# Kernel tuning notes

Measured on AMD Instinct MI355X. Metric: run time of the kernel, lower is better.

## Reference

```python
import jax, jax.numpy as jnp
import numpy as np

B, T, D, H = 64, 512, 512, 1024


def setup_inputs() -> dict:
    key = jax.random.key(0)
    k_x, k_m, k_wi, k_wh = jax.random.split(key, 4)
    x = jax.random.normal(k_x, (B, T, D), dtype=jnp.float32)
    mask = jax.random.randint(k_m, (B, T), 0, 2, dtype=jnp.int32)
    # LSTMCell params: xavier_uniform for W_ih, orthogonal for W_hh, zero biases
    lim = float(np.sqrt(6.0 / (4 * H + D)))
    W_ih = jax.random.uniform(k_wi, (4 * H, D), dtype=jnp.float32, minval=-lim, maxval=lim)
    A = jax.random.normal(k_wh, (4 * H, H), dtype=jnp.float32)
    Q, _ = jnp.linalg.qr(A.T)  # (H, 4H) columns orthonormal -> rows of W_hh orthogonal-ish per torch init
    W_hh = Q.T.astype(jnp.float32)
    W_hh = jnp.concatenate([W_hh] * ((4 * H) // W_hh.shape[0]), axis=0)[: 4 * H]
    b_ih = jnp.zeros((4 * H,), dtype=jnp.float32)
    b_hh = jnp.zeros((4 * H,), dtype=jnp.float32)
    h0 = jnp.zeros((1, H), dtype=jnp.float32)
    c0 = jnp.zeros((1, H), dtype=jnp.float32)
    return {"x": x, "mask": mask, "W_ih": W_ih, "W_hh": W_hh,
            "b_ih": b_ih, "b_hh": b_hh, "h0": h0, "c0": c0}


def reference(x, mask, W_ih, W_hh, b_ih, b_hh, h0, c0):
    Bn, Tn, _ = x.shape
    Hn = h0.shape[1]
    # Precompute input projection for all timesteps: (B, T, 4H)
    xg = jnp.einsum('btd,gd->btg', x, W_ih) + b_ih + b_hh

    def step(carry, inp):
        h, c = carry
        xg_t, m_t = inp  # (B, 4H), (B,)
        gates = xg_t + h @ W_hh.T  # (B, 4H)
        i, f, g, o = jnp.split(gates, 4, axis=-1)  # torch LSTMCell gate order i,f,g,o
        i = jax.nn.sigmoid(i)
        f = jax.nn.sigmoid(f)
        g = jnp.tanh(g)
        o = jax.nn.sigmoid(o)
        c_new = f * c + i * g
        h_new = o * jnp.tanh(c_new)
        keep = (m_t != 0)[:, None]
        h2 = jnp.where(keep, h_new, h)
        c2 = jnp.where(keep, c_new, c)
        return (h2, c2), h2

    h_init = jnp.broadcast_to(h0, (Bn, Hn))
    c_init = jnp.broadcast_to(c0, (Bn, Hn))
    xs = (jnp.swapaxes(xg, 0, 1), mask.T)  # time-major for scan
    (_, _), hs = jax.lax.scan(step, (h_init, c_init), xs)
    return jnp.swapaxes(hs, 0, 1)  # (B, T, H)
```

## Files before the change

kernel.cpp:

```cpp
#include <hip/hip_runtime.h>

#define B_   64
#define T_   512
#define D_   512
#define H_   1024
#define G4   4096
#define KC_N 48

typedef float f32x4 __attribute__((ext_vector_type(4)));
typedef short s16x8 __attribute__((ext_vector_type(8)));

__device__ __forceinline__ unsigned short f2bf(float f) {
    unsigned int u = __float_as_uint(f);
    u = (u + 0x7fffu + ((u >> 16) & 1u)) >> 16;
    return (unsigned short)u;
}
__device__ __forceinline__ float sigm(float x) { return 1.f / (1.f + __expf(-x)); }
__device__ __forceinline__ float tanh_f(float x) { return 1.f - 2.f / (__expf(2.f * x) + 1.f); }

__device__ __forceinline__ s16x8 cvt8(float4 a, float4 b) {
    union { s16x8 v; unsigned int u[4]; } r;
    asm("v_cvt_pk_bf16_f32 %0, %1, %2" : "=v"(r.u[0]) : "v"(a.x), "v"(a.y));
    asm("v_cvt_pk_bf16_f32 %0, %1, %2" : "=v"(r.u[1]) : "v"(a.z), "v"(a.w));
    asm("v_cvt_pk_bf16_f32 %0, %1, %2" : "=v"(r.u[2]) : "v"(b.x), "v"(b.y));
    asm("v_cvt_pk_bf16_f32 %0, %1, %2" : "=v"(r.u[3]) : "v"(b.z), "v"(b.w));
    return r.v;
}

__global__ __launch_bounds__(256) void pack_w(const float* __restrict__ W_ih,
                                              const float* __restrict__ W_hh,
                                              unsigned short* __restrict__ Wpk) {
    int tid = blockIdx.x * 256 + threadIdx.x;
    int j    = tid & 7;
    int lane = (tid >> 3) & 63;
    int rest = tid >> 9;
    int kc = rest % KC_N;
    int c  = rest / KC_N;
    int npk = c * 16 + (lane & 15);
    int jh = npk >> 2, g = npk & 3;
    int row = g * H_ + jh;
    int k = kc * 32 + (lane >> 4) * 8 + j;
    float v = (k < D_) ? W_ih[row * D_ + k] : W_hh[row * H_ + (k - D_)];
    Wpk[tid] = f2bf(v);
}

__global__ __launch_bounds__(256) void init_state2(
    const float* __restrict__ h0, const float* __restrict__ b_ih,
    const float* __restrict__ b_hh, unsigned short* __restrict__ hbuf,
    float* __restrict__ bias_p, unsigned int* __restrict__ flags)
{
    int tid = blockIdx.x * 256 + threadIdx.x;
    int j = tid & (H_ - 1);
    hbuf[tid] = f2bf(h0[j]);
    if (tid < G4) {
        int jh = tid >> 2, g = tid & 3;
        bias_p[tid] = b_ih[g * H_ + jh] + b_hh[g * H_ + jh];
    }
    if (tid < 256) flags[tid] = 0u;
}

__global__ __launch_bounds__(512) void lstm_persist(
    const float* __restrict__ x, const int* __restrict__ mask,
    const unsigned short* __restrict__ Wpk, const float* __restrict__ bias_p,
    const float* __restrict__ h0, const float* __restrict__ c0,
    unsigned short* __restrict__ hbuf, float* __restrict__ out,
    unsigned int* __restrict__ flags)
{
    const int tid = threadIdx.x;
    const int bid = blockIdx.x;
    const int cg  = bid >> 1;
    const int mh  = bid & 1;
    const int b0g = mh << 5;

    const int w = tid >> 6, l = tid & 63;
    const int quad = l >> 4, l15 = l & 15;
    const int mi = w >> 2;
    const int ks = w & 3;
    const int arow = b0g + mi * 16 + l15;

    __shared__ float Dls[4][32][36];

    s16x8 Bf0[12], Bf1[12];
    {
        const unsigned short* base0 = Wpk + (size_t)((cg * 2 + 0) * KC_N) * 512;
        const unsigned short* base1 = Wpk + (size_t)((cg * 2 + 1) * KC_N) * 512;
        #pragma unroll
        for (int i = 0; i < 12; ++i) {
            int kc = (i < 4) ? (ks * 4 + i) : (16 + ks * 8 + (i - 4));
            Bf0[i] = *reinterpret_cast<const s16x8*>(base0 + ((size_t)kc * 64 + l) * 8);
            Bf1[i] = *reinterpret_cast<const s16x8*>(base1 + ((size_t)kc * 64 + l) * 8);
        }
        #pragma unroll
        for (int i = 0; i < 12; ++i)
            asm volatile("" : "+v"(Bf0[i]), "+v"(Bf1[i]));
    }

    const int b_l = tid >> 3, u = tid & 7;
    const int brow = b0g + b_l;
    const int jcol = cg * 8 + u;
    float c_reg = 0.f, h_reg = 0.f;
    float4 bias = make_float4(0.f, 0.f, 0.f, 0.f);
    if (tid < 256) {
        c_reg = c0[jcol];
        h_reg = h0[jcol];
        bias = *reinterpret_cast<const float4*>(bias_p + cg * 32 + u * 4);
    }

    unsigned int* myflag = flags + mh * 128 + cg;
    const unsigned long long* pollp =
        reinterpret_cast<const unsigned long long*>(flags + mh * 128) + l;
    const float* xbase = x + (size_t)arow * T_ * D_ + ks * 128 + quad * 8;

    #pragma unroll 1
    for (int t = 0; t < T_; ++t) {
        const unsigned short* hin  = hbuf + (size_t)(t & 1) * (B_ * H_);
        unsigned short*       hout = hbuf + (size_t)((t + 1) & 1) * (B_ * H_);

        f32x4 a0 = {0.f, 0.f, 0.f, 0.f}, a1 = {0.f, 0.f, 0.f, 0.f};
        const float* xp = xbase + (size_t)t * D_;
        int mv = 0;
        if (tid < 256) mv = mask[(size_t)brow * T_ + t];
        #pragma unroll
        for (int i = 0; i < 4; ++i) {
            float4 v0 = *reinterpret_cast<const float4*>(xp + i * 32);
            float4 v1 = *reinterpret_cast<const float4*>(xp + i * 32 + 4);
            s16x8 af = cvt8(v0, v1);
            a0 = __builtin_amdgcn_mfma_f32_16x16x32_bf16(af, Bf0[i], a0, 0, 0, 0);
            a1 = __builtin_amdgcn_mfma_f32_16x16x32_bf16(af, Bf1[i], a1, 0, 0, 0);
        }

        if (t > 0 && w == 0) {
            const unsigned int tgt = (unsigned int)t;
            int guard = 0;
            for (;;) {
                unsigned long long v = __hip_atomic_load(pollp, __ATOMIC_RELAXED,
                                                         __HIP_MEMORY_SCOPE_AGENT);
                int ok = ((unsigned int)v >= tgt) && ((unsigned int)(v >> 32) >= tgt);
                if (__all(ok)) break;
                __builtin_amdgcn_s_sleep(2);
                if (++guard > (1 << 16)) break;
            }
        }
        __builtin_amdgcn_s_barrier();
        __builtin_amdgcn_fence(__ATOMIC_ACQUIRE, "workgroup");

        const unsigned short* hrow = hin + (size_t)arow * H_ + ks * 256 + quad * 8;
        s16x8 hf[8];
        #pragma unroll
        for (int i = 0; i < 8; ++i) {
            const unsigned long long* hp =
                reinterpret_cast<const unsigned long long*>(hrow + i * 32);
            union { s16x8 v; unsigned long long q[2]; } au;
            au.q[0] = __hip_atomic_load(hp,     __ATOMIC_RELAXED, __HIP_MEMORY_SCOPE_AGENT);
            au.q[1] = __hip_atomic_load(hp + 1, __ATOMIC_RELAXED, __HIP_MEMORY_SCOPE_AGENT);
            hf[i] = au.v;
        }
        #pragma unroll
        for (int i = 0; i < 8; ++i) {
            a0 = __builtin_amdgcn_mfma_f32_16x16x32_bf16(hf[i], Bf0[4 + i], a0, 0, 0, 0);
            a1 = __builtin_amdgcn_mfma_f32_16x16x32_bf16(hf[i], Bf1[4 + i], a1, 0, 0, 0);
        }
        #pragma unroll
        for (int r = 0; r < 4; ++r) {
            Dls[ks][mi * 16 + quad * 4 + r][l15]      = a0[r];
            Dls[ks][mi * 16 + quad * 4 + r][16 + l15] = a1[r];
        }
        __syncthreads();

        float h2s = 0.f;
        if (tid < 256) {
            f32x4 s0 = *reinterpret_cast<f32x4*>(&Dls[0][b_l][u * 4]);
            f32x4 s1 = *reinterpret_cast<f32x4*>(&Dls[1][b_l][u * 4]);
            f32x4 s2 = *reinterpret_cast<f32x4*>(&Dls[2][b_l][u * 4]);
            f32x4 s3 = *reinterpret_cast<f32x4*>(&Dls[3][b_l][u * 4]);
            f32x4 g = s0 + s1 + s2 + s3;
            float gi = sigm  (g[0] + bias.x);
            float gf = sigm  (g[1] + bias.y);
            float gg = tanh_f(g[2] + bias.z);
            float go = sigm  (g[3] + bias.w);
            float c_new = gf * c_reg + gi * gg;
            float h_new = go * tanh_f(c_new);
            float h2 = mv ? h_new : h_reg;
            c_reg = mv ? c_new : c_reg;
            h_reg = h2;
            h2s = h2;
            unsigned int hv = (unsigned int)f2bf(h2);
            unsigned int hx = (unsigned int)__shfl_xor((int)hv, 1);
            if ((u & 1) == 0) {
                unsigned int pk = (hx << 16) | hv;
                __hip_atomic_store(reinterpret_cast<unsigned int*>(
                                       hout + (size_t)brow * H_ + jcol),
                                   pk, __ATOMIC_RELAXED, __HIP_MEMORY_SCOPE_AGENT);
            }
        }
        __syncthreads();

        if (t < T_ - 1 && tid == 0)
            __hip_atomic_store(myflag, (unsigned int)(t + 1),
                               __ATOMIC_RELAXED, __HIP_MEMORY_SCOPE_AGENT);
        if (tid < 256)
            out[((size_t)brow * T_ + t) * H_ + jcol] = h2s;
    }
}

extern "C" void kernel_launch(void* const* d_in, const int* in_sizes, int n_in,
                              void* d_out, int out_size, void* d_ws, size_t ws_size,
                              hipStream_t stream)
{
    const float* x    = (const float*)d_in[0];
    const int*   mask = (const int*)d_in[1];
    const float* W_ih = (const float*)d_in[2];
    const float* W_hh = (const float*)d_in[3];
    const float* b_ih = (const float*)d_in[4];
    const float* b_hh = (const float*)d_in[5];
    const float* h0   = (const float*)d_in[6];
    const float* c0   = (const float*)d_in[7];
    float* out = (float*)d_out;

    char* wsb = (char*)d_ws;
    unsigned short* Wpk    = (unsigned short*)(wsb);
    float*          bias_p = (float*)(wsb + 12582912);
    unsigned short* hbuf   = (unsigned short*)(wsb + 12599296);
    unsigned int*   flags  = (unsigned int*)(wsb + 12861440);

    pack_w<<<24576, 256, 0, stream>>>(W_ih, W_hh, Wpk);
    init_state2<<<256, 256, 0, stream>>>(h0, b_ih, b_hh, hbuf, bias_p, flags);
    lstm_persist<<<256, 512, 0, stream>>>(x, mask, Wpk, bias_p, h0, c0, hbuf, out, flags);
}
```

Before: 3.749 ms.

## Halve persistent grid to 128 blocks, each covering 16 hidden units

Result: slower. 4.366 ms (+16.5%).

```diff
diff --git a/kernel.cpp b/kernel.cpp
--- a/kernel.cpp
+++ b/kernel.cpp
@@ -59,7 +59,7 @@
     if (tid < 256) flags[tid] = 0u;
 }
 
-__global__ __launch_bounds__(512) void lstm_persist(
+__global__ __launch_bounds__(512, 2) void lstm_persist(
     const float* __restrict__ x, const int* __restrict__ mask,
     const unsigned short* __restrict__ Wpk, const float* __restrict__ bias_p,
     const float* __restrict__ h0, const float* __restrict__ c0,
@@ -68,7 +68,7 @@
 {
     const int tid = threadIdx.x;
     const int bid = blockIdx.x;
-    const int cg  = bid >> 1;
+    const int cgB = bid >> 1;
     const int mh  = bid & 1;
     const int b0g = mh << 5;
 
@@ -78,65 +78,69 @@
     const int ks = w & 3;
     const int arow = b0g + mi * 16 + l15;
 
-    __shared__ float Dls[4][32][36];
-
-    s16x8 Bf0[12], Bf1[12];
-    {
-        const unsigned short* base0 = Wpk + (size_t)((cg * 2 + 0) * KC_N) * 512;
-        const unsigned short* base1 = Wpk + (size_t)((cg * 2 + 1) * KC_N) * 512;
-        #pragma unroll
-        for (int i = 0; i < 12; ++i) {
-            int kc = (i < 4) ? (ks * 4 + i) : (16 + ks * 8 + (i - 4));
-            Bf0[i] = *reinterpret_cast<const s16x8*>(base0 + ((size_t)kc * 64 + l) * 8);
-            Bf1[i] = *reinterpret_cast<const s16x8*>(base1 + ((size_t)kc * 64 + l) * 8);
-        }
-        #pragma unroll
-        for (int i = 0; i < 12; ++i)
-            asm volatile("" : "+v"(Bf0[i]), "+v"(Bf1[i]));
+    __shared__ float Dls[4][32][68];
+
+    s16x8 Bh[4][8];
+    #pragma unroll
+    for (int nt = 0; nt < 4; ++nt) {
+        const unsigned short* cb = Wpk + (size_t)(cgB * 4 + nt) * (KC_N * 512);
+        #pragma unroll
+        for (int i = 0; i < 8; ++i) {
+            int kc = 16 + ks * 8 + i;
+            Bh[nt][i] = *reinterpret_cast<const s16x8*>(cb + (size_t)kc * 512 + l * 8);
+        }
     }
-
-    const int b_l = tid >> 3, u = tid & 7;
+    #pragma unroll
+    for (int nt = 0; nt < 4; ++nt)
+        #pragma unroll
+        for (int i = 0; i < 8; ++i)
+            asm volatile("" : "+v"(Bh[nt][i]));
+
+    const int b_l = tid >> 4, u = tid & 15;
     const int brow = b0g + b_l;
-    const int jcol = cg * 8 + u;
-    float c_reg = 0.f, h_reg = 0.f;
-    float4 bias = make_float4(0.f, 0.f, 0.f, 0.f);
-    if (tid < 256) {
-        c_reg = c0[jcol];
-        h_reg = h0[jcol];
-        bias = *reinterpret_cast<const float4*>(bias_p + cg * 32 + u * 4);
-    }
-
-    unsigned int* myflag = flags + mh * 128 + cg;
-    const unsigned long long* pollp =
-        reinterpret_cast<const unsigned long long*>(flags + mh * 128) + l;
+    const int jcol = cgB * 16 + u;
+    float c_reg = c0[jcol];
+    float h_reg = h0[jcol];
+    float4 bias = *reinterpret_cast<const float4*>(bias_p + cgB * 64 + u * 4);
+
+    unsigned int* myflag = flags + mh * 64 + cgB;
+    const unsigned int* pollp = flags + mh * 64 + l;
     const float* xbase = x + (size_t)arow * T_ * D_ + ks * 128 + quad * 8;
+    const unsigned short* wxb = Wpk + (size_t)(cgB * 4) * (KC_N * 512) + (size_t)l * 8;
 
     #pragma unroll 1
     for (int t = 0; t < T_; ++t) {
         const unsigned short* hin  = hbuf + (size_t)(t & 1) * (B_ * H_);
         unsigned short*       hout = hbuf + (size_t)((t + 1) & 1) * (B_ * H_);
 
-        f32x4 a0 = {0.f, 0.f, 0.f, 0.f}, a1 = {0.f, 0.f, 0.f, 0.f};
+        f32x4 acc[4];
+        #pragma unroll
+        for (int nt = 0; nt < 4; ++nt) acc[nt] = (f32x4){0.f, 0.f, 0.f, 0.f};
         const float* xp = xbase + (size_t)t * D_;
-        int mv = 0;
-        if (tid < 256) mv = mask[(size_t)brow * T_ + t];
+        int mv = mask[(size_t)brow * T_ + t];
         #pragma unroll
         for (int i = 0; i < 4; ++i) {
+            int kc = ks * 4 + i;
+            s16x8 bx0 = *reinterpret_cast<const s16x8*>(wxb + ((size_t)0 * KC_N + kc) * 512);
+            s16x8 bx1 = *reinterpret_cast<const s16x8*>(wxb + ((size_t)1 * KC_N + kc) * 512);
+            s16x8 bx2 = *reinterpret_cast<const s16x8*>(wxb + ((size_t)2 * KC_N + kc) * 512);
+            s16x8 bx3 = *reinterpret_cast<const s16x8*>(wxb + ((size_t)3 * KC_N + kc) * 512);
             float4 v0 = *reinterpret_cast<const float4*>(xp + i * 32);
             float4 v1 = *reinterpret_cast<const float4*>(xp + i * 32 + 4);
             s16x8 af = cvt8(v0, v1);
-            a0 = __builtin_amdgcn_mfma_f32_16x16x32_bf16(af, Bf0[i], a0, 0, 0, 0);
-            a1 = __builtin_amdgcn_mfma_f32_16x16x32_bf16(af, Bf1[i], a1, 0, 0, 0);
+            acc[0] = __builtin_amdgcn_mfma_f32_16x16x32_bf16(af, bx0, acc[0], 0, 0, 0);
+            acc[1] = __builtin_amdgcn_mfma_f32_16x16x32_bf16(af, bx1, acc[1], 0, 0, 0);
+            acc[2] = __builtin_amdgcn_mfma_f32_16x16x32_bf16(af, bx2, acc[2], 0, 0, 0);
+            acc[3] = __builtin_amdgcn_mfma_f32_16x16x32_bf16(af, bx3, acc[3], 0, 0, 0);
         }
 
         if (t > 0 && w == 0) {
             const unsigned int tgt = (unsigned int)t;
             int guard = 0;
             for (;;) {
-                unsigned long long v = __hip_atomic_load(pollp, __ATOMIC_RELAXED,
-                                                         __HIP_MEMORY_SCOPE_AGENT);
-                int ok = ((unsigned int)v >= tgt) && ((unsigned int)(v >> 32) >= tgt);
-                if (__all(ok)) break;
+                unsigned int v = __hip_atomic_load(pollp, __ATOMIC_RELAXED,
+                                                   __HIP_MEMORY_SCOPE_AGENT);
+                if (__all((int)(v >= tgt))) break;
                 __builtin_amdgcn_s_sleep(2);
                 if (++guard > (1 << 16)) break;
             }
@@ -157,49 +161,48 @@
         }
         #pragma unroll
         for (int i = 0; i < 8; ++i) {
-            a0 = __builtin_amdgcn_mfma_f32_16x16x32_bf16(hf[i], Bf0[4 + i], a0, 0, 0, 0);
-            a1 = __builtin_amdgcn_mfma_f32_16x16x32_bf16(hf[i], Bf1[4 + i], a1, 0, 0, 0);
+            acc[0] = __builtin_amdgcn_mfma_f32_16x16x32_bf16(hf[i], Bh[0][i], acc[0], 0, 0, 0);
+            acc[1] = __builtin_amdgcn_mfma_f32_16x16x32_bf16(hf[i], Bh[1][i], acc[1], 0, 0, 0);
+            acc[2] = __builtin_amdgcn_mfma_f32_16x16x32_bf16(hf[i], Bh[2][i], acc[2], 0, 0, 0);
+            acc[3] = __builtin_amdgcn_mfma_f32_16x16x32_bf16(hf[i], Bh[3][i], acc[3], 0, 0, 0);
         }
         #pragma unroll
         for (int r = 0; r < 4; ++r) {
-            Dls[ks][mi * 16 + quad * 4 + r][l15]      = a0[r];
-            Dls[ks][mi * 16 + quad * 4 + r][16 + l15] = a1[r];
+            Dls[ks][mi * 16 + quad * 4 + r][l15]      = acc[0][r];
+            Dls[ks][mi * 16 + quad * 4 + r][16 + l15] = acc[1][r];
+            Dls[ks][mi * 16 + quad * 4 + r][32 + l15] = acc[2][r];
+            Dls[ks][mi * 16 + quad * 4 + r][48 + l15] = acc[3][r];
         }
         __syncthreads();
 
-        float h2s = 0.f;
-        if (tid < 256) {
-            f32x4 s0 = *reinterpret_cast<f32x4*>(&Dls[0][b_l][u * 4]);
-            f32x4 s1 = *reinterpret_cast<f32x4*>(&Dls[1][b_l][u * 4]);
-            f32x4 s2 = *reinterpret_cast<f32x4*>(&Dls[2][b_l][u * 4]);
-            f32x4 s3 = *reinterpret_cast<f32x4*>(&Dls[3][b_l][u * 4]);
-            f32x4 g = s0 + s1 + s2 + s3;
-            float gi = sigm  (g[0] + bias.x);
-            float gf = sigm  (g[1] + bias.y);
-            float gg = tanh_f(g[2] + bias.z);
-            float go = sigm  (g[3] + bias.w);
-            float c_new = gf * c_reg + gi * gg;
-            float h_new = go * tanh_f(c_new);
-            float h2 = mv ? h_new : h_reg;
-            c_reg = mv ? c_new : c_reg;
-            h_reg = h2;
-            h2s = h2;
-            unsigned int hv = (unsigned int)f2bf(h2);
-            unsigned int hx = (unsigned int)__shfl_xor((int)hv, 1);
-            if ((u & 1) == 0) {
-                unsigned int pk = (hx << 16) | hv;
-                __hip_atomic_store(reinterpret_cast<unsigned int*>(
-                                       hout + (size_t)brow * H_ + jcol),
-                                   pk, __ATOMIC_RELAXED, __HIP_MEMORY_SCOPE_AGENT);
-            }
+        f32x4 s0 = *reinterpret_cast<f32x4*>(&Dls[0][b_l][u * 4]);
+        f32x4 s1 = *reinterpret_cast<f32x4*>(&Dls[1][b_l][u * 4]);
+        f32x4 s2 = *reinterpret_cast<f32x4*>(&Dls[2][b_l][u * 4]);
+        f32x4 s3 = *reinterpret_cast<f32x4*>(&Dls[3][b_l][u * 4]);
+        f32x4 g = s0 + s1 + s2 + s3;
+        float gi = sigm  (g[0] + bias.x);
+        float gf = sigm  (g[1] + bias.y);
+        float gg = tanh_f(g[2] + bias.z);
+        float go = sigm  (g[3] + bias.w);
+        float c_new = gf * c_reg + gi * gg;
+        float h_new = go * tanh_f(c_new);
+        float h2 = mv ? h_new : h_reg;
+        c_reg = mv ? c_new : c_reg;
+        h_reg = h2;
+        unsigned int hv = (unsigned int)f2bf(h2);
+        unsigned int hx = (unsigned int)__shfl_xor((int)hv, 1);
+        if ((u & 1) == 0) {
+            unsigned int pk = (hx << 16) | hv;
+            __hip_atomic_store(reinterpret_cast<unsigned int*>(
+                                   hout + (size_t)brow * H_ + jcol),
+                               pk, __ATOMIC_RELAXED, __HIP_MEMORY_SCOPE_AGENT);
         }
         __syncthreads();
 
         if (t < T_ - 1 && tid == 0)
             __hip_atomic_store(myflag, (unsigned int)(t + 1),
                                __ATOMIC_RELAXED, __HIP_MEMORY_SCOPE_AGENT);
-        if (tid < 256)
-            out[((size_t)brow * T_ + t) * H_ + jcol] = h2s;
+        out[((size_t)brow * T_ + t) * H_ + jcol] = h2;
     }
 }
 
@@ -225,5 +228,5 @@
 
     pack_w<<<24576, 256, 0, stream>>>(W_ih, W_hh, Wpk);
     init_state2<<<256, 256, 0, stream>>>(h0, b_ih, b_hh, hbuf, bias_p, flags);
-    lstm_persist<<<256, 512, 0, stream>>>(x, mask, Wpk, bias_p, h0, c0, hbuf, out, flags);
-}
+    lstm_persist<<<128, 512, 0, stream>>>(x, mask, Wpk, bias_p, h0, c0, hbuf, out, flags);
+}
```

## Replace per-block flag polling with tagged hidden-state words for synchronization

Applied to the files above, without the earlier changes.

After: 5.284 ms. 1.41x slower.

```diff
diff --git a/kernel.cpp b/kernel.cpp
--- a/kernel.cpp
+++ b/kernel.cpp
@@ -46,25 +46,23 @@
 
 __global__ __launch_bounds__(256) void init_state2(
     const float* __restrict__ h0, const float* __restrict__ b_ih,
-    const float* __restrict__ b_hh, unsigned short* __restrict__ hbuf,
-    float* __restrict__ bias_p, unsigned int* __restrict__ flags)
+    const float* __restrict__ b_hh, unsigned int* __restrict__ hbuf32,
+    float* __restrict__ bias_p)
 {
     int tid = blockIdx.x * 256 + threadIdx.x;
     int j = tid & (H_ - 1);
-    hbuf[tid] = f2bf(h0[j]);
+    hbuf32[tid] = ((unsigned int)f2bf(h0[j]) << 16);
     if (tid < G4) {
         int jh = tid >> 2, g = tid & 3;
         bias_p[tid] = b_ih[g * H_ + jh] + b_hh[g * H_ + jh];
     }
-    if (tid < 256) flags[tid] = 0u;
 }
 
 __global__ __launch_bounds__(512) void lstm_persist(
     const float* __restrict__ x, const int* __restrict__ mask,
     const unsigned short* __restrict__ Wpk, const float* __restrict__ bias_p,
     const float* __restrict__ h0, const float* __restrict__ c0,
-    unsigned short* __restrict__ hbuf, float* __restrict__ out,
-    unsigned int* __restrict__ flags)
+    unsigned int* __restrict__ hbuf32, float* __restrict__ out)
 {
     const int tid = threadIdx.x;
     const int bid = blockIdx.x;
@@ -106,15 +104,12 @@
         bias = *reinterpret_cast<const float4*>(bias_p + cg * 32 + u * 4);
     }
 
-    unsigned int* myflag = flags + mh * 128 + cg;
-    const unsigned long long* pollp =
-        reinterpret_cast<const unsigned long long*>(flags + mh * 128) + l;
     const float* xbase = x + (size_t)arow * T_ * D_ + ks * 128 + quad * 8;
 
     #pragma unroll 1
     for (int t = 0; t < T_; ++t) {
-        const unsigned short* hin  = hbuf + (size_t)(t & 1) * (B_ * H_);
-        unsigned short*       hout = hbuf + (size_t)((t + 1) & 1) * (B_ * H_);
+        const unsigned int* hin32  = hbuf32 + (size_t)(t & 1) * (B_ * H_);
+        unsigned int*       hout32 = hbuf32 + (size_t)((t + 1) & 1) * (B_ * H_);
 
         f32x4 a0 = {0.f, 0.f, 0.f, 0.f}, a1 = {0.f, 0.f, 0.f, 0.f};
         const float* xp = xbase + (size_t)t * D_;
@@ -129,31 +124,44 @@
             a1 = __builtin_amdgcn_mfma_f32_16x16x32_bf16(af, Bf1[i], a1, 0, 0, 0);
         }
 
-        if (t > 0 && w == 0) {
-            const unsigned int tgt = (unsigned int)t;
+        const unsigned int* hrowf = hin32 + (size_t)arow * H_ + ks * 256 + quad * 8;
+        const unsigned int tag = (unsigned int)t & 0xffffu;
+        s16x8 hf[8];
+        {
             int guard = 0;
             for (;;) {
-                unsigned long long v = __hip_atomic_load(pollp, __ATOMIC_RELAXED,
-                                                         __HIP_MEMORY_SCOPE_AGENT);
-                int ok = ((unsigned int)v >= tgt) && ((unsigned int)(v >> 32) >= tgt);
-                if (__all(ok)) break;
-                __builtin_amdgcn_s_sleep(2);
-                if (++guard > (1 << 16)) break;
+                unsigned long long q[32];
+                #pragma unroll
+                for (int i = 0; i < 8; ++i) {
+                    const unsigned long long* p =
+                        reinterpret_cast<const unsigned long long*>(hrowf + i * 32);
+                    q[i*4+0] = __hip_atomic_load(p+0, __ATOMIC_RELAXED, __HIP_MEMORY_SCOPE_AGENT);
+                    q[i*4+1] = __hip_atomic_load(p+1, __ATOMIC_RELAXED, __HIP_MEMORY_SCOPE_AGENT);
+                    q[i*4+2] = __hip_atomic_load(p+2, __ATOMIC_RELAXED, __HIP_MEMORY_SCOPE_AGENT);
+                    q[i*4+3] = __hip_atomic_load(p+3, __ATOMIC_RELAXED, __HIP_MEMORY_SCOPE_AGENT);
+                }
+                int ok = 1;
+                #pragma unroll
+                for (int i = 0; i < 32; ++i)
+                    ok &= (int)((((unsigned int)q[i] & 0xffffu) == tag) &
+                                (((unsigned int)(q[i] >> 32) & 0xffffu) == tag));
+                ++guard;
+                if (__all(ok) || guard > 20000) {
+                    #pragma unroll
+                    for (int i = 0; i < 8; ++i) {
+                        union { s16x8 v; unsigned int d[4]; } fu;
+                        #pragma unroll
+                        for (int d4 = 0; d4 < 4; ++d4) {
+                            unsigned long long wq = q[i*4 + d4];
+                            fu.d[d4] = ((unsigned int)(wq >> 32) & 0xffff0000u) |
+                                       ((unsigned int)wq >> 16);
+                        }
+                        hf[i] = fu.v;
+                    }
+                    break;
+                }
+                __builtin_amdgcn_s_sleep(4);
             }
-        }
-        __builtin_amdgcn_s_barrier();
-        __builtin_amdgcn_fence(__ATOMIC_ACQUIRE, "workgroup");
-
-        const unsigned short* hrow = hin + (size_t)arow * H_ + ks * 256 + quad * 8;
-        s16x8 hf[8];
-        #pragma unroll
-        for (int i = 0; i < 8; ++i) {
-            const unsigned long long* hp =
-                reinterpret_cast<const unsigned long long*>(hrow + i * 32);
-            union { s16x8 v; unsigned long long q[2]; } au;
-            au.q[0] = __hip_atomic_load(hp,     __ATOMIC_RELAXED, __HIP_MEMORY_SCOPE_AGENT);
-            au.q[1] = __hip_atomic_load(hp + 1, __ATOMIC_RELAXED, __HIP_MEMORY_SCOPE_AGENT);
-            hf[i] = au.v;
         }
         #pragma unroll
         for (int i = 0; i < 8; ++i) {
@@ -167,7 +175,6 @@
         }
         __syncthreads();
 
-        float h2s = 0.f;
         if (tid < 256) {
             f32x4 s0 = *reinterpret_cast<f32x4*>(&Dls[0][b_l][u * 4]);
             f32x4 s1 = *reinterpret_cast<f32x4*>(&Dls[1][b_l][u * 4]);
@@ -183,23 +190,15 @@
             float h2 = mv ? h_new : h_reg;
             c_reg = mv ? c_new : c_reg;
             h_reg = h2;
-            h2s = h2;
-            unsigned int hv = (unsigned int)f2bf(h2);
-            unsigned int hx = (unsigned int)__shfl_xor((int)hv, 1);
-            if ((u & 1) == 0) {
-                unsigned int pk = (hx << 16) | hv;
-                __hip_atomic_store(reinterpret_cast<unsigned int*>(
-                                       hout + (size_t)brow * H_ + jcol),
-                                   pk, __ATOMIC_RELAXED, __HIP_MEMORY_SCOPE_AGENT);
+            if (t < T_ - 1) {
+                unsigned int wv = ((unsigned int)f2bf(h2) << 16) |
+                                  ((unsigned int)(t + 1) & 0xffffu);
+                __hip_atomic_store(hout32 + (size_t)brow * H_ + jcol, wv,
+                                   __ATOMIC_RELAXED, __HIP_MEMORY_SCOPE_AGENT);
             }
+            out[((size_t)brow * T_ + t) * H_ + jcol] = h2;
         }
         __syncthreads();
-
-        if (t < T_ - 1 && tid == 0)
-            __hip_atomic_store(myflag, (unsigned int)(t + 1),
-                               __ATOMIC_RELAXED, __HIP_MEMORY_SCOPE_AGENT);
-        if (tid < 256)
-            out[((size_t)brow * T_ + t) * H_ + jcol] = h2s;
     }
 }
 
@@ -220,10 +219,9 @@
     char* wsb = (char*)d_ws;
     unsigned short* Wpk    = (unsigned short*)(wsb);
     float*          bias_p = (float*)(wsb + 12582912);
-    unsigned short* hbuf   = (unsigned short*)(wsb + 12599296);
-    unsigned int*   flags  = (unsigned int*)(wsb + 12861440);
+    unsigned int*   hbuf32 = (unsigned int*)(wsb + 12599296);
 
     pack_w<<<24576, 256, 0, stream>>>(W_ih, W_hh, Wpk);
-    init_state2<<<256, 256, 0, stream>>>(h0, b_ih, b_hh, hbuf, bias_p, flags);
-    lstm_persist<<<256, 512, 0, stream>>>(x, mask, Wpk, bias_p, h0, c0, hbuf, out, flags);
-}
+    init_state2<<<512, 256, 0, stream>>>(h0, b_ih, b_hh, hbuf32, bias_p);
+    lstm_persist<<<256, 512, 0, stream>>>(x, mask, Wpk, bias_p, h0, c0, hbuf32, out);
+}
```
